# Kernel tuning notes

Hardware: AMD Instinct MI355X
Metric: run time of the kernel (lower is better)

The kernel has to match this reference:

```python
import jax, jax.numpy as jnp
import numpy as np

D_MODEL = 1024
N_HEADS = 16
D_K = D_MODEL // N_HEADS


def setup_inputs() -> dict:
    key = jax.random.key(0)
    ks = jax.random.split(key, 11)
    B, S = 2, 2048
    scale = 1.0 / np.sqrt(D_MODEL)
    inp = {
        "q": jax.random.normal(ks[0], (B, S, D_MODEL), jnp.float32),
        "k": jax.random.normal(ks[1], (B, S, D_MODEL), jnp.float32),
        "v": jax.random.normal(ks[2], (B, S, D_MODEL), jnp.float32),
        "W_q": jax.random.normal(ks[3], (D_MODEL, D_MODEL), jnp.float32) * scale,
        "b_q": jnp.zeros((D_MODEL,), jnp.float32),
        "W_k": jax.random.normal(ks[4], (D_MODEL, D_MODEL), jnp.float32) * scale,
        "b_k": jnp.zeros((D_MODEL,), jnp.float32),
        "W_v": jax.random.normal(ks[5], (D_MODEL, D_MODEL), jnp.float32) * scale,
        "b_v": jnp.zeros((D_MODEL,), jnp.float32),
        "W_o": jax.random.normal(ks[6], (D_MODEL, D_MODEL), jnp.float32) * scale,
        "b_o": jnp.zeros((D_MODEL,), jnp.float32),
    }
    return inp


def _split_heads(x):
    B, S, _ = x.shape
    return x.reshape(B, S, N_HEADS, D_K).transpose(0, 2, 1, 3)  # [B,H,S,dk]


def reference(q, k, v, W_q, b_q, W_k, b_k, W_v, b_v, W_o, b_o):
    Q = _split_heads(q @ W_q + b_q)
    K = _split_heads(k @ W_k + b_k)
    V = _split_heads(v @ W_v + b_v)
    scores = jnp.einsum("bhqd,bhkd->bhqk", Q, K) / jnp.sqrt(jnp.float32(D_K))
    attn = jax.nn.softmax(scores, axis=-1)  # [B,H,S,S]
    out = jnp.einsum("bhqk,bhkd->bhqd", attn, V)
    B, H, S, dk = out.shape
    out = out.transpose(0, 2, 1, 3).reshape(B, S, H * dk)
    return out @ W_o + b_o, attn
```

## Files before the change

kernel.cpp:

```cpp
#include <hip/hip_runtime.h>
#include <hip/hip_bf16.h>

typedef __bf16 bf16x8 __attribute__((ext_vector_type(8)));
typedef float f32x4 __attribute__((ext_vector_type(4)));
typedef short short4v __attribute__((ext_vector_type(4)));
typedef unsigned short ushort8v __attribute__((ext_vector_type(8)));

#define DEV static __device__ __forceinline__

#if __has_builtin(__builtin_amdgcn_exp2f)
#define EXP2(x) __builtin_amdgcn_exp2f(x)
#else
#define EXP2(x) exp2f(x)
#endif

DEV unsigned short f2bf(float x) {
  union { __hip_bfloat16 b; unsigned short u; } c;
  c.b = __float2bfloat16(x);
  return c.u;
}

DEV unsigned f2bf_fast_u(float x) {
  union { float f; unsigned u; } c;
  c.f = x;
  return (c.u + 0x7fff + ((c.u >> 16) & 1)) >> 16;
}
DEV unsigned short f2bf_fast(float x) { return (unsigned short)f2bf_fast_u(x); }

DEV void gload_lds16(const void* g, void* l) {
  __builtin_amdgcn_global_load_lds((const __attribute__((address_space(1))) void*)g,
                                   (__attribute__((address_space(3))) void*)l, 16, 0, 0);
}

__global__ __launch_bounds__(256) void cvt_qkv(const float* __restrict__ q,
                                               const float* __restrict__ k,
                                               const float* __restrict__ v,
                                               unsigned short* __restrict__ qb,
                                               unsigned short* __restrict__ kb,
                                               unsigned short* __restrict__ vb) {
  const float* src = blockIdx.y == 0 ? q : (blockIdx.y == 1 ? k : v);
  unsigned short* dst = blockIdx.y == 0 ? qb : (blockIdx.y == 1 ? kb : vb);
  int idx = (blockIdx.x * 256 + threadIdx.x) * 4;
  float4 xv = *(const float4*)(src + idx);
  ushort4 o;
  o.x = f2bf(xv.x); o.y = f2bf(xv.y); o.z = f2bf(xv.z); o.w = f2bf(xv.w);
  *(ushort4*)(dst + idx) = o;
}

__global__ __launch_bounds__(256) void transpose_all(const float* __restrict__ W0,
                                                     const float* __restrict__ W1,
                                                     const float* __restrict__ W2,
                                                     const float* __restrict__ W3,
                                                     unsigned short* __restrict__ T0,
                                                     unsigned short* __restrict__ T1,
                                                     unsigned short* __restrict__ T2,
                                                     unsigned short* __restrict__ T3) {
  __shared__ float t[64][68];
  int sel = blockIdx.x >> 8;
  const float* W = sel == 0 ? W0 : sel == 1 ? W1 : sel == 2 ? W2 : W3;
  unsigned short* Wt = sel == 0 ? T0 : sel == 1 ? T1 : sel == 2 ? T2 : T3;
  int tile = blockIdx.x & 255;
  int tr = tile >> 4, tc = tile & 15;
  int lr = threadIdx.x >> 4, lc4 = threadIdx.x & 15;
#pragma unroll
  for (int i = 0; i < 4; ++i) {
    int r = i * 16 + lr;
    float4 v = *(const float4*)(W + (size_t)(tr * 64 + r) * 1024 + tc * 64 + lc4 * 4);
    t[r][lc4 * 4 + 0] = v.x; t[r][lc4 * 4 + 1] = v.y;
    t[r][lc4 * 4 + 2] = v.z; t[r][lc4 * 4 + 3] = v.w;
  }
  __syncthreads();
#pragma unroll
  for (int i = 0; i < 4; ++i) {
    int r = i * 16 + lr;
    ushort4 o;
    o.x = f2bf(t[lc4 * 4 + 0][r]);
    o.y = f2bf(t[lc4 * 4 + 1][r]);
    o.z = f2bf(t[lc4 * 4 + 2][r]);
    o.w = f2bf(t[lc4 * 4 + 3][r]);
    *(ushort4*)(Wt + (size_t)(tc * 64 + r) * 1024 + tr * 64 + lc4 * 4) = o;
  }
}

DEV void gemm_core(const unsigned short* __restrict__ A, const unsigned short* __restrict__ Bt,
                   const float* __restrict__ bias, void* __restrict__ Cout,
                   float scale, int mode, int blk,
                   unsigned short* As, unsigned short* Bs) {
  const int tid = threadIdx.x;
  const int l = tid & 63, w = tid >> 6;
  const int wm = w >> 1, wn = w & 1;
  const int r15 = l & 15, kg = l >> 4;
  const int mt = blk >> 3, nt = blk & 7;

  const f32x4 fz = {0.f, 0.f, 0.f, 0.f};
  f32x4 acc[4][4];
#pragma unroll
  for (int i = 0; i < 4; ++i)
#pragma unroll
    for (int j = 0; j < 4; ++j) acc[i][j] = fz;

  for (int kt = 0; kt < 16; ++kt) {
#pragma unroll
    for (int c = 0; c < 4; ++c) {
      int chunk = c * 256 + tid;
      int row = chunk >> 3, slot = chunk & 7;
      int gsl = slot ^ (row & 7);
      gload_lds16(A + (size_t)(mt * 128 + row) * 1024 + kt * 64 + gsl * 8, As + chunk * 8);
      gload_lds16(Bt + (size_t)(nt * 128 + row) * 1024 + kt * 64 + gsl * 8, Bs + chunk * 8);
    }
    __syncthreads();
#pragma unroll
    for (int ks = 0; ks < 2; ++ks) {
      bf16x8 a[4], b[4];
      int slot = ks * 4 + kg;
#pragma unroll
      for (int i = 0; i < 4; ++i) {
        int ra = wm * 64 + i * 16 + r15;
        a[i] = *(const bf16x8*)(As + ra * 64 + (slot ^ (ra & 7)) * 8);
        int rb = wn * 64 + i * 16 + r15;
        b[i] = *(const bf16x8*)(Bs + rb * 64 + (slot ^ (rb & 7)) * 8);
      }
#pragma unroll
      for (int i = 0; i < 4; ++i)
#pragma unroll
        for (int j = 0; j < 4; ++j)
          acc[i][j] = __builtin_amdgcn_mfma_f32_16x16x32_bf16(a[i], b[j], acc[i][j], 0, 0, 0);
    }
    __syncthreads();
  }

#pragma unroll
  for (int j = 0; j < 4; ++j) {
    int gc = nt * 128 + wn * 64 + j * 16 + r15;
    float bj = bias[gc];
#pragma unroll
    for (int i = 0; i < 4; ++i) {
#pragma unroll
      for (int r = 0; r < 4; ++r) {
        int gr = mt * 128 + wm * 64 + i * 16 + kg * 4 + r;
        float val = (acc[i][j][r] + bj) * scale;
        if (mode == 2) {
          ((float*)Cout)[(size_t)gr * 1024 + gc] = val;
        } else {
          int bb = gr >> 11, s = gr & 2047, hh = gc >> 6, dk = gc & 63;
          if (mode == 0)
            ((unsigned short*)Cout)[((size_t)(bb * 16 + hh) * 2048 + s) * 64 + dk] = f2bf(val);
          else
            ((unsigned short*)Cout)[((size_t)(bb * 16 + hh) * 64 + dk) * 2048 + s] = f2bf(val);
        }
      }
    }
  }
}

__global__ __launch_bounds__(256) void gemm_qkv(const unsigned short* __restrict__ qb,
                                                const unsigned short* __restrict__ kb,
                                                const unsigned short* __restrict__ vb,
                                                const unsigned short* __restrict__ Wtq,
                                                const unsigned short* __restrict__ Wtk,
                                                const unsigned short* __restrict__ Wtv,
                                                const float* __restrict__ bq,
                                                const float* __restrict__ bk,
                                                const float* __restrict__ bv,
                                                unsigned short* __restrict__ Qh,
                                                unsigned short* __restrict__ Kh,
                                                unsigned short* __restrict__ Vt) {
  __shared__ unsigned short As[128 * 64];
  __shared__ unsigned short Bs[128 * 64];
  int sel = blockIdx.x >> 8, blk = blockIdx.x & 255;
  const unsigned short* A = sel == 0 ? qb : sel == 1 ? kb : vb;
  const unsigned short* Bt = sel == 0 ? Wtq : sel == 1 ? Wtk : Wtv;
  const float* bias = sel == 0 ? bq : sel == 1 ? bk : bv;
  void* C = sel == 0 ? (void*)Qh : sel == 1 ? (void*)Kh : (void*)Vt;
  gemm_core(A, Bt, bias, C, sel == 0 ? 0.125f * 1.44269504088896f : 1.0f,
            sel == 2 ? 1 : 0, blk, As, Bs);
}

__global__ __launch_bounds__(256) void gemm_out(const unsigned short* __restrict__ AO,
                                                const unsigned short* __restrict__ Wto,
                                                const float* __restrict__ bo,
                                                float* __restrict__ out0) {
  __shared__ unsigned short As[128 * 64];
  __shared__ unsigned short Bs[128 * 64];
  gemm_core(AO, Wto, bo, out0, 1.0f, 2, blockIdx.x, As, Bs);
}

__global__ __launch_bounds__(256) void attn_flash(const unsigned short* __restrict__ Qh,
                                                  const unsigned short* __restrict__ Kh,
                                                  const unsigned short* __restrict__ Vt,
                                                  unsigned short* __restrict__ AO,
                                                  float* __restrict__ rrowG) {
  __shared__ float Ored[4][32][68];
  __shared__ float Ss[4][32];
  __shared__ float rrow[32];

  const int tid = threadIdx.x;
  const int l = tid & 63, w = tid >> 6;
  const int r15 = l & 15, kg = l >> 4;

  const int lb = ((int)blockIdx.x & 7) * 256 + ((int)blockIdx.x >> 3);
  const int bh = lb >> 6;
  const int q0 = (lb & 63) * 32;
  const int b = bh >> 4, h = bh & 15;

  const unsigned short* Kbase = Kh + (size_t)bh * 2048 * 64;
  const unsigned short* Vbase = Vt + (size_t)bh * 64 * 2048;

  bf16x8 aq[2][2];
#pragma unroll
  for (int j = 0; j < 2; ++j)
#pragma unroll
    for (int h2 = 0; h2 < 2; ++h2)
      aq[j][h2] = *(const bf16x8*)(Qh + ((size_t)bh * 2048 + q0 + j * 16 + r15) * 64 +
                                   (h2 * 4 + kg) * 8);

  const f32x4 z4 = {0.f, 0.f, 0.f, 0.f};
  float s2[2] = {0.f, 0.f};
  f32x4 oacc[2][4];
#pragma unroll
  for (int j = 0; j < 2; ++j)
#pragma unroll
    for (int d = 0; d < 4; ++d) oacc[j][d] = z4;

  const int kb0 = w * 16;
  for (int kt = 0; kt < 32; ++kt) {
    const unsigned short* kp = Kbase + (size_t)(kt * 64 + kb0 + r15) * 64;
    bf16x8 kf0 = *(const bf16x8*)(kp + kg * 8);
    bf16x8 kf1 = *(const bf16x8*)(kp + 32 + kg * 8);
    short4v vf[4];
#pragma unroll
    for (int d = 0; d < 4; ++d)
      vf[d] = *(const short4v*)(Vbase + (size_t)(d * 16 + r15) * 2048 + kt * 64 + kb0 + kg * 4);
#pragma unroll
    for (int j = 0; j < 2; ++j) {
      f32x4 sc = __builtin_amdgcn_mfma_f32_16x16x32_bf16(kf0, aq[j][0], z4, 0, 0, 0);
      sc = __builtin_amdgcn_mfma_f32_16x16x32_bf16(kf1, aq[j][1], sc, 0, 0, 0);
      float e0 = EXP2(sc[0]), e1 = EXP2(sc[1]), e2 = EXP2(sc[2]), e3 = EXP2(sc[3]);
      s2[j] += (e0 + e1) + (e2 + e3);
      short4v pf;
      pf[0] = (short)f2bf_fast(e0); pf[1] = (short)f2bf_fast(e1);
      pf[2] = (short)f2bf_fast(e2); pf[3] = (short)f2bf_fast(e3);
#pragma unroll
      for (int d = 0; d < 4; ++d)
        oacc[j][d] = __builtin_amdgcn_mfma_f32_16x16x16bf16_1k(vf[d], pf, oacc[j][d], 0, 0, 0);
    }
  }

#pragma unroll
  for (int j = 0; j < 2; ++j) {
    s2[j] += __shfl_xor(s2[j], 16, 64);
    s2[j] += __shfl_xor(s2[j], 32, 64);
    if (kg == 0) Ss[w][j * 16 + r15] = s2[j];
  }
  __syncthreads();
  if (tid < 32) {
    float s = Ss[0][tid] + Ss[1][tid] + Ss[2][tid] + Ss[3][tid];
    float rv = 1.0f / s;
    rrow[tid] = rv;
    rrowG[(size_t)bh * 2048 + q0 + tid] = rv;
  }
  __syncthreads();

#pragma unroll
  for (int j = 0; j < 2; ++j)
#pragma unroll
    for (int d = 0; d < 4; ++d)
      *(f32x4*)&Ored[w][j * 16 + r15][d * 16 + kg * 4] = oacc[j][d];
  __syncthreads();
  {
    int q = tid >> 3, dc = (tid & 7) * 8;
    float rv = rrow[q];
    ushort8v o;
#pragma unroll
    for (int i = 0; i < 8; ++i) {
      float s = Ored[0][q][dc + i] + Ored[1][q][dc + i] + Ored[2][q][dc + i] + Ored[3][q][dc + i];
      o[i] = f2bf(s * rv);
    }
    *(ushort8v*)(AO + ((size_t)(b * 2048 + q0 + q)) * 1024 + h * 64 + dc) = o;
  }
}

__global__ __launch_bounds__(256) void attn_write(const unsigned short* __restrict__ Qh,
                                                  const unsigned short* __restrict__ Kh,
                                                  const float* __restrict__ rrowG,
                                                  float* __restrict__ attnO) {
  __shared__ unsigned short Pl[16 * 2048];

  const int tid = threadIdx.x;
  const int l = tid & 63, w = tid >> 6;
  const int r15 = l & 15, kg = l >> 4;

  const int lb = ((int)blockIdx.x & 7) * 512 + ((int)blockIdx.x >> 3);
  const int bh = lb >> 7;
  const int q0 = (lb & 127) * 16;

  const unsigned short* Kbase = Kh + (size_t)bh * 2048 * 64;
  const unsigned short* Qp = Qh + ((size_t)bh * 2048 + q0 + r15) * 64;
  bf16x8 aq0 = *(const bf16x8*)(Qp + kg * 8);
  bf16x8 aq1 = *(const bf16x8*)(Qp + 32 + kg * 8);

  const float lrv = __log2f(rrowG[(size_t)bh * 2048 + q0 + r15]);

  const f32x4 z4 = {0.f, 0.f, 0.f, 0.f};
  const int kq = w * 512;
  char* Plb = (char*)Pl;

  bf16x8 ka[4][2], kb[4][2];

#define LOADK(KF, c)                                                              \
  {                                                                               \
    const unsigned short* kp_ = Kbase + (size_t)(kq + (c) * 64 + r15) * 64 + kg * 8; \
    _Pragma("unroll")                                                             \
    for (int sub = 0; sub < 4; ++sub) {                                           \
      KF[sub][0] = *(const bf16x8*)(kp_ + sub * 16 * 64);                         \
      KF[sub][1] = *(const bf16x8*)(kp_ + sub * 16 * 64 + 32);                    \
    }                                                                             \
  }

#define PROCESS(KF, c)                                                            \
  {                                                                               \
    _Pragma("unroll")                                                             \
    for (int sub = 0; sub < 4; ++sub) {                                           \
      f32x4 sc = __builtin_amdgcn_mfma_f32_16x16x32_bf16(KF[sub][0], aq0, z4, 0, 0, 0); \
      sc = __builtin_amdgcn_mfma_f32_16x16x32_bf16(KF[sub][1], aq1, sc, 0, 0, 0); \
      unsigned u0 = f2bf_fast_u(EXP2(sc[0] + lrv)) | (f2bf_fast_u(EXP2(sc[1] + lrv)) << 16); \
      unsigned u1 = f2bf_fast_u(EXP2(sc[2] + lrv)) | (f2bf_fast_u(EXP2(sc[3] + lrv)) << 16); \
      int colb = (kq + (c) * 64 + sub * 16 + kg * 4) * 2;                         \
      uint2 uu = {u0, u1};                                                        \
      *(uint2*)(Plb + r15 * 4096 + (colb ^ ((r15 & 7) << 4))) = uu;               \
    }                                                                             \
  }

  LOADK(ka, 0)
  for (int c = 0; c < 8; c += 2) {
    LOADK(kb, c + 1)
    PROCESS(ka, c)
    if (c + 2 < 8) LOADK(ka, c + 2)
    PROCESS(kb, c + 1)
  }
#undef LOADK
#undef PROCESS

  __syncthreads();

  float* wavep = attnO + ((size_t)bh * 2048 + q0 + w * 4) * 2048;
#pragma unroll
  for (int ri = 0; ri < 4; ++ri) {
    int qr = w * 4 + ri;
    const char* rowl = Plb + qr * 4096;
    int swz = (qr & 7) << 4;
    float* rowp = wavep + (size_t)ri * 2048 + l * 4;
#pragma unroll
    for (int seg = 0; seg < 8; ++seg) {
      uint2 u = *(const uint2*)(rowl + ((seg * 512 + l * 8) ^ swz));
      union { unsigned u; float f; } c0, c1, c2, c3;
      c0.u = u.x << 16; c1.u = u.x & 0xffff0000u;
      c2.u = u.y << 16; c3.u = u.y & 0xffff0000u;
      f32x4 v = {c0.f, c1.f, c2.f, c3.f};
      __builtin_nontemporal_store(v, (f32x4*)(rowp + seg * 256));
    }
  }
}

extern "C" void kernel_launch(void* const* d_in, const int* in_sizes, int n_in,
                              void* d_out, int out_size, void* d_ws, size_t ws_size,
                              hipStream_t stream) {
  const float* q  = (const float*)d_in[0];
  const float* k  = (const float*)d_in[1];
  const float* v  = (const float*)d_in[2];
  const float* Wq = (const float*)d_in[3];
  const float* bq = (const float*)d_in[4];
  const float* Wk = (const float*)d_in[5];
  const float* bk = (const float*)d_in[6];
  const float* Wv = (const float*)d_in[7];
  const float* bvp = (const float*)d_in[8];
  const float* Wo = (const float*)d_in[9];
  const float* bo = (const float*)d_in[10];

  char* wsb = (char*)d_ws;
  const size_t MB = (size_t)1 << 20;
  unsigned short* qb  = (unsigned short*)(wsb + 0 * MB);
  unsigned short* kbp = (unsigned short*)(wsb + 8 * MB);
  unsigned short* vbp = (unsigned short*)(wsb + 16 * MB);
  unsigned short* Wtq = (unsigned short*)(wsb + 24 * MB);
  unsigned short* Wtk = (unsigned short*)(wsb + 26 * MB);
  unsigned short* Wtv = (unsigned short*)(wsb + 28 * MB);
  unsigned short* Wto = (unsigned short*)(wsb + 30 * MB);
  unsigned short* Qh  = (unsigned short*)(wsb + 32 * MB);
  unsigned short* Kh  = (unsigned short*)(wsb + 40 * MB);
  unsigned short* Vt  = (unsigned short*)(wsb + 48 * MB);
  unsigned short* AO  = (unsigned short*)(wsb + 56 * MB);
  float* rrowG = (float*)(wsb + 0 * MB);

  float* attnO = (float*)d_out + (size_t)2 * 2048 * 1024;

  cvt_qkv<<<dim3(4096, 3), 256, 0, stream>>>(q, k, v, qb, kbp, vbp);
  transpose_all<<<1024, 256, 0, stream>>>(Wq, Wk, Wv, Wo, Wtq, Wtk, Wtv, Wto);
  gemm_qkv<<<768, 256, 0, stream>>>(qb, kbp, vbp, Wtq, Wtk, Wtv, bq, bk, bvp, Qh, Kh, Vt);
  attn_flash<<<2048, 256, 0, stream>>>(Qh, Kh, Vt, AO, rrowG);
  attn_write<<<4096, 256, 0, stream>>>(Qh, Kh, rrowG, attnO);
  gemm_out<<<256, 256, 0, stream>>>(AO, Wto, bo, (float*)d_out);
}
```

Before: 412.7 us.

## Fuse flash attention and attention-matrix write into one kernel

Merges the two attention kernels so each block computes QK^T once, keeps the unnormalized bf16 probabilities in LDS, accumulates PV, then writes the normalized attention matrix and the head output. This removes the second QK^T and exp pass, the rrowG round trip and one kernel launch. In exchange each block handles 16 queries instead of 32, so V is reloaded twice as often. Register pressure from the double-buffered V fragments is higher and could reduce occupancy.

```diff
diff --git a/kernel.cpp b/kernel.cpp
--- a/kernel.cpp
+++ b/kernel.cpp
@@ -185,127 +185,42 @@
   gemm_core(AO, Wto, bo, out0, 1.0f, 2, blockIdx.x, As, Bs);
 }
 
-__global__ __launch_bounds__(256) void attn_flash(const unsigned short* __restrict__ Qh,
+__global__ __launch_bounds__(256) void attn_fused(const unsigned short* __restrict__ Qh,
                                                   const unsigned short* __restrict__ Kh,
                                                   const unsigned short* __restrict__ Vt,
-                                                  unsigned short* __restrict__ AO,
-                                                  float* __restrict__ rrowG) {
-  __shared__ float Ored[4][32][68];
-  __shared__ float Ss[4][32];
-  __shared__ float rrow[32];
+                                                  float* __restrict__ attnO,
+                                                  unsigned short* __restrict__ AO) {
+  __shared__ __align__(16) char smem[65536];
+  __shared__ float Ss[4][16];
+  __shared__ float rrow[16];
 
   const int tid = threadIdx.x;
   const int l = tid & 63, w = tid >> 6;
   const int r15 = l & 15, kg = l >> 4;
 
-  const int lb = ((int)blockIdx.x & 7) * 256 + ((int)blockIdx.x >> 3);
-  const int bh = lb >> 6;
-  const int q0 = (lb & 63) * 32;
-  const int b = bh >> 4, h = bh & 15;
-
-  const unsigned short* Kbase = Kh + (size_t)bh * 2048 * 64;
-  const unsigned short* Vbase = Vt + (size_t)bh * 64 * 2048;
-
-  bf16x8 aq[2][2];
-#pragma unroll
-  for (int j = 0; j < 2; ++j)
-#pragma unroll
-    for (int h2 = 0; h2 < 2; ++h2)
-      aq[j][h2] = *(const bf16x8*)(Qh + ((size_t)bh * 2048 + q0 + j * 16 + r15) * 64 +
-                                   (h2 * 4 + kg) * 8);
-
-  const f32x4 z4 = {0.f, 0.f, 0.f, 0.f};
-  float s2[2] = {0.f, 0.f};
-  f32x4 oacc[2][4];
-#pragma unroll
-  for (int j = 0; j < 2; ++j)
-#pragma unroll
-    for (int d = 0; d < 4; ++d) oacc[j][d] = z4;
-
-  const int kb0 = w * 16;
-  for (int kt = 0; kt < 32; ++kt) {
-    const unsigned short* kp = Kbase + (size_t)(kt * 64 + kb0 + r15) * 64;
-    bf16x8 kf0 = *(const bf16x8*)(kp + kg * 8);
-    bf16x8 kf1 = *(const bf16x8*)(kp + 32 + kg * 8);
-    short4v vf[4];
-#pragma unroll
-    for (int d = 0; d < 4; ++d)
-      vf[d] = *(const short4v*)(Vbase + (size_t)(d * 16 + r15) * 2048 + kt * 64 + kb0 + kg * 4);
-#pragma unroll
-    for (int j = 0; j < 2; ++j) {
-      f32x4 sc = __builtin_amdgcn_mfma_f32_16x16x32_bf16(kf0, aq[j][0], z4, 0, 0, 0);
-      sc = __builtin_amdgcn_mfma_f32_16x16x32_bf16(kf1, aq[j][1], sc, 0, 0, 0);
-      float e0 = EXP2(sc[0]), e1 = EXP2(sc[1]), e2 = EXP2(sc[2]), e3 = EXP2(sc[3]);
-      s2[j] += (e0 + e1) + (e2 + e3);
-      short4v pf;
-      pf[0] = (short)f2bf_fast(e0); pf[1] = (short)f2bf_fast(e1);
-      pf[2] = (short)f2bf_fast(e2); pf[3] = (short)f2bf_fast(e3);
-#pragma unroll
-      for (int d = 0; d < 4; ++d)
-        oacc[j][d] = __builtin_amdgcn_mfma_f32_16x16x16bf16_1k(vf[d], pf, oacc[j][d], 0, 0, 0);
-    }
-  }
-
-#pragma unroll
-  for (int j = 0; j < 2; ++j) {
-    s2[j] += __shfl_xor(s2[j], 16, 64);
-    s2[j] += __shfl_xor(s2[j], 32, 64);
-    if (kg == 0) Ss[w][j * 16 + r15] = s2[j];
-  }
-  __syncthreads();
-  if (tid < 32) {
-    float s = Ss[0][tid] + Ss[1][tid] + Ss[2][tid] + Ss[3][tid];
-    float rv = 1.0f / s;
-    rrow[tid] = rv;
-    rrowG[(size_t)bh * 2048 + q0 + tid] = rv;
-  }
-  __syncthreads();
-
-#pragma unroll
-  for (int j = 0; j < 2; ++j)
-#pragma unroll
-    for (int d = 0; d < 4; ++d)
-      *(f32x4*)&Ored[w][j * 16 + r15][d * 16 + kg * 4] = oacc[j][d];
-  __syncthreads();
-  {
-    int q = tid >> 3, dc = (tid & 7) * 8;
-    float rv = rrow[q];
-    ushort8v o;
-#pragma unroll
-    for (int i = 0; i < 8; ++i) {
-      float s = Ored[0][q][dc + i] + Ored[1][q][dc + i] + Ored[2][q][dc + i] + Ored[3][q][dc + i];
-      o[i] = f2bf(s * rv);
-    }
-    *(ushort8v*)(AO + ((size_t)(b * 2048 + q0 + q)) * 1024 + h * 64 + dc) = o;
-  }
-}
-
-__global__ __launch_bounds__(256) void attn_write(const unsigned short* __restrict__ Qh,
-                                                  const unsigned short* __restrict__ Kh,
-                                                  const float* __restrict__ rrowG,
-                                                  float* __restrict__ attnO) {
-  __shared__ unsigned short Pl[16 * 2048];
-
-  const int tid = threadIdx.x;
-  const int l = tid & 63, w = tid >> 6;
-  const int r15 = l & 15, kg = l >> 4;
-
   const int lb = ((int)blockIdx.x & 7) * 512 + ((int)blockIdx.x >> 3);
   const int bh = lb >> 7;
   const int q0 = (lb & 127) * 16;
+  const int b = bh >> 4, h = bh & 15;
 
   const unsigned short* Kbase = Kh + (size_t)bh * 2048 * 64;
+  const unsigned short* Vbase = Vt + (size_t)bh * 64 * 2048;
+
   const unsigned short* Qp = Qh + ((size_t)bh * 2048 + q0 + r15) * 64;
   bf16x8 aq0 = *(const bf16x8*)(Qp + kg * 8);
   bf16x8 aq1 = *(const bf16x8*)(Qp + 32 + kg * 8);
 
-  const float lrv = __log2f(rrowG[(size_t)bh * 2048 + q0 + r15]);
-
   const f32x4 z4 = {0.f, 0.f, 0.f, 0.f};
   const int kq = w * 512;
-  char* Plb = (char*)Pl;
+  char* Plb = smem;
+
+  float s2 = 0.f;
+  f32x4 oacc[4];
+#pragma unroll
+  for (int d = 0; d < 4; ++d) oacc[d] = z4;
 
   bf16x8 ka[4][2], kb[4][2];
+  short4v va[4][4], vb_[4][4];
 
 #define LOADK(KF, c)                                                              \
   {                                                                               \
@@ -317,30 +232,53 @@
     }                                                                             \
   }
 
-#define PROCESS(KF, c)                                                            \
+#define LOADV(VF, c)                                                              \
+  {                                                                               \
+    const unsigned short* vp_ = Vbase + (size_t)r15 * 2048 + kq + (c) * 64 + kg * 4; \
+    _Pragma("unroll")                                                             \
+    for (int sub = 0; sub < 4; ++sub)                                             \
+      _Pragma("unroll")                                                           \
+      for (int d = 0; d < 4; ++d)                                                 \
+        VF[sub][d] = *(const short4v*)(vp_ + (size_t)d * 16 * 2048 + sub * 16);   \
+  }
+
+#define PROCESS(KF, VF, c)                                                        \
   {                                                                               \
     _Pragma("unroll")                                                             \
     for (int sub = 0; sub < 4; ++sub) {                                           \
       f32x4 sc = __builtin_amdgcn_mfma_f32_16x16x32_bf16(KF[sub][0], aq0, z4, 0, 0, 0); \
       sc = __builtin_amdgcn_mfma_f32_16x16x32_bf16(KF[sub][1], aq1, sc, 0, 0, 0); \
-      unsigned u0 = f2bf_fast_u(EXP2(sc[0] + lrv)) | (f2bf_fast_u(EXP2(sc[1] + lrv)) << 16); \
-      unsigned u1 = f2bf_fast_u(EXP2(sc[2] + lrv)) | (f2bf_fast_u(EXP2(sc[3] + lrv)) << 16); \
+      float e0 = EXP2(sc[0]), e1 = EXP2(sc[1]), e2 = EXP2(sc[2]), e3 = EXP2(sc[3]); \
+      s2 += (e0 + e1) + (e2 + e3);                                                \
+      unsigned p0 = f2bf_fast_u(e0), p1 = f2bf_fast_u(e1);                        \
+      unsigned p2 = f2bf_fast_u(e2), p3 = f2bf_fast_u(e3);                        \
       int colb = (kq + (c) * 64 + sub * 16 + kg * 4) * 2;                         \
-      uint2 uu = {u0, u1};                                                        \
+      uint2 uu = {p0 | (p1 << 16), p2 | (p3 << 16)};                              \
       *(uint2*)(Plb + r15 * 4096 + (colb ^ ((r15 & 7) << 4))) = uu;               \
+      short4v pf;                                                                 \
+      pf[0] = (short)p0; pf[1] = (short)p1; pf[2] = (short)p2; pf[3] = (short)p3; \
+      _Pragma("unroll")                                                           \
+      for (int d = 0; d < 4; ++d)                                                 \
+        oacc[d] = __builtin_amdgcn_mfma_f32_16x16x16bf16_1k(VF[sub][d], pf, oacc[d], 0, 0, 0); \
     }                                                                             \
   }
 
-  LOADK(ka, 0)
+  LOADK(ka, 0) LOADV(va, 0)
   for (int c = 0; c < 8; c += 2) {
-    LOADK(kb, c + 1)
-    PROCESS(ka, c)
-    if (c + 2 < 8) LOADK(ka, c + 2)
-    PROCESS(kb, c + 1)
+    LOADK(kb, c + 1) LOADV(vb_, c + 1)
+    PROCESS(ka, va, c)
+    if (c + 2 < 8) { LOADK(ka, c + 2) LOADV(va, c + 2) }
+    PROCESS(kb, vb_, c + 1)
   }
 #undef LOADK
+#undef LOADV
 #undef PROCESS
 
+  s2 += __shfl_xor(s2, 16, 64);
+  s2 += __shfl_xor(s2, 32, 64);
+  if (kg == 0) Ss[w][r15] = s2;
+  __syncthreads();
+  if (tid < 16) rrow[tid] = 1.0f / (Ss[0][tid] + Ss[1][tid] + Ss[2][tid] + Ss[3][tid]);
   __syncthreads();
 
   float* wavep = attnO + ((size_t)bh * 2048 + q0 + w * 4) * 2048;
@@ -349,6 +287,7 @@
     int qr = w * 4 + ri;
     const char* rowl = Plb + qr * 4096;
     int swz = (qr & 7) << 4;
+    float rv = rrow[qr];
     float* rowp = wavep + (size_t)ri * 2048 + l * 4;
 #pragma unroll
     for (int seg = 0; seg < 8; ++seg) {
@@ -356,9 +295,28 @@
       union { unsigned u; float f; } c0, c1, c2, c3;
       c0.u = u.x << 16; c1.u = u.x & 0xffff0000u;
       c2.u = u.y << 16; c3.u = u.y & 0xffff0000u;
-      f32x4 v = {c0.f, c1.f, c2.f, c3.f};
+      f32x4 v = {c0.f * rv, c1.f * rv, c2.f * rv, c3.f * rv};
       __builtin_nontemporal_store(v, (f32x4*)(rowp + seg * 256));
     }
+  }
+  __syncthreads();
+
+  float (*Ored)[16][68] = (float (*)[16][68])smem;
+#pragma unroll
+  for (int d = 0; d < 4; ++d)
+    *(f32x4*)&Ored[w][r15][d * 16 + kg * 4] = oacc[d];
+  __syncthreads();
+  {
+    int q = tid >> 4, dc = (tid & 15) * 4;
+    float rv = rrow[q];
+    ushort4 o;
+    float v0 = Ored[0][q][dc + 0] + Ored[1][q][dc + 0] + Ored[2][q][dc + 0] + Ored[3][q][dc + 0];
+    float v1 = Ored[0][q][dc + 1] + Ored[1][q][dc + 1] + Ored[2][q][dc + 1] + Ored[3][q][dc + 1];
+    float v2 = Ored[0][q][dc + 2] + Ored[1][q][dc + 2] + Ored[2][q][dc + 2] + Ored[3][q][dc + 2];
+    float v3 = Ored[0][q][dc + 3] + Ored[1][q][dc + 3] + Ored[2][q][dc + 3] + Ored[3][q][dc + 3];
+    o.x = f2bf(v0 * rv); o.y = f2bf(v1 * rv);
+    o.z = f2bf(v2 * rv); o.w = f2bf(v3 * rv);
+    *(ushort4*)(AO + ((size_t)(b * 2048 + q0 + q)) * 1024 + h * 64 + dc) = o;
   }
 }
 
@@ -390,14 +348,12 @@
   unsigned short* Kh  = (unsigned short*)(wsb + 40 * MB);
   unsigned short* Vt  = (unsigned short*)(wsb + 48 * MB);
   unsigned short* AO  = (unsigned short*)(wsb + 56 * MB);
-  float* rrowG = (float*)(wsb + 0 * MB);
 
   float* attnO = (float*)d_out + (size_t)2 * 2048 * 1024;
 
   cvt_qkv<<<dim3(4096, 3), 256, 0, stream>>>(q, k, v, qb, kbp, vbp);
   transpose_all<<<1024, 256, 0, stream>>>(Wq, Wk, Wv, Wo, Wtq, Wtk, Wtv, Wto);
   gemm_qkv<<<768, 256, 0, stream>>>(qb, kbp, vbp, Wtq, Wtk, Wtv, bq, bk, bvp, Qh, Kh, Vt);
-  attn_flash<<<2048, 256, 0, stream>>>(Qh, Kh, Vt, AO, rrowG);
-  attn_write<<<4096, 256, 0, stream>>>(Qh, Kh, rrowG, attnO);
+  attn_fused<<<4096, 256, 0, stream>>>(Qh, Kh, Vt, attnO, AO);
   gemm_out<<<256, 256, 0, stream>>>(AO, Wto, bo, (float*)d_out);
 }
```

After: 457.7 us. 10.9% more time.
